# Optimization experiments

Measured on AMD Instinct MI355X. Metric: run time of the kernel, lower is better.

The kernel has to match this reference:

```python
import jax, jax.numpy as jnp
import numpy as np

N = 100000
E = 1600000
F_IN = 64
F_OUT = 64
C = 1.0
MIN_NORM = 1e-15
BALL_EPS = 4e-3  # float32 eps in HGCN PoincareBall.proj


def _norm(x):
    return jnp.clip(jnp.linalg.norm(x, axis=-1, keepdims=True), MIN_NORM)


def artanh(x):
    return jnp.arctanh(jnp.clip(x, -1.0 + 1e-7, 1.0 - 1e-7))


def proj(x, c):
    # project back onto the Poincare ball of curvature -c
    norm = _norm(x)
    maxnorm = (1.0 - BALL_EPS) / jnp.sqrt(c)
    return jnp.where(norm > maxnorm, x / norm * maxnorm, x)


def mobius_matvec(m, x, c):
    sqrt_c = jnp.sqrt(c)
    x_norm = _norm(x)
    mx = x @ m.T
    mx_norm = _norm(mx)
    res = jnp.tanh(mx_norm / x_norm * artanh(sqrt_c * x_norm)) * mx / (mx_norm * sqrt_c)
    zero_mx = jnp.all(mx == 0, axis=-1, keepdims=True)
    return jnp.where(zero_mx, jnp.zeros_like(res), res)


def expmap0(u, c):
    sqrt_c = jnp.sqrt(c)
    u_norm = _norm(u)
    return jnp.tanh(sqrt_c * u_norm) * u / (sqrt_c * u_norm)


def mobius_add(x, y, c):
    x2 = jnp.sum(x * x, axis=-1, keepdims=True)
    y2 = jnp.sum(y * y, axis=-1, keepdims=True)
    xy = jnp.sum(x * y, axis=-1, keepdims=True)
    num = (1.0 + 2.0 * c * xy + c * y2) * x + (1.0 - c * x2) * y
    denom = 1.0 + 2.0 * c * xy + c * c * x2 * y2
    return num / jnp.clip(denom, MIN_NORM)


def hyp_linear(x, W, b, c):
    res = proj(mobius_matvec(W, x, c), c)
    if b is not None:
        hyp_bias = proj(expmap0(b[None, :], c), c)
        res = proj(mobius_add(res, hyp_bias, c), c)
    return res


def scatter_mean(edge_index, x, n):
    # mean of source features over edges landing at each target node; 0 if isolated
    src, dst = edge_index[0], edge_index[1]
    s = jax.ops.segment_sum(x[src], dst, num_segments=n)
    cnt = jax.ops.segment_sum(jnp.ones((src.shape[0], 1), x.dtype), dst, num_segments=n)
    return s / jnp.clip(cnt, 1.0)


def setup_inputs() -> dict:
    key = jax.random.key(0)
    ks = jax.random.split(key, 9)
    glorot = 1.0 / np.sqrt(F_IN)
    return {
        "x": jax.random.normal(ks[0], (N, F_IN), dtype=jnp.float32) * 0.1,
        "W_pos": jax.random.uniform(ks[1], (F_OUT, F_IN), jnp.float32, -glorot, glorot),
        "W_pos_cc": jax.random.uniform(ks[2], (F_OUT, F_IN), jnp.float32, -glorot, glorot),
        "b_pos_cc": jax.random.uniform(ks[3], (F_OUT,), jnp.float32, -glorot, glorot),
        "W_neg": jax.random.uniform(ks[4], (F_OUT, F_IN), jnp.float32, -glorot, glorot),
        "W_neg_cc": jax.random.uniform(ks[5], (F_OUT, F_IN), jnp.float32, -glorot, glorot),
        "b_neg_cc": jax.random.uniform(ks[6], (F_OUT,), jnp.float32, -glorot, glorot),
        "pos_edge_index": jax.random.randint(ks[7], (2, E), 0, N, dtype=jnp.int64) if jax.config.jax_enable_x64 else jax.random.randint(ks[7], (2, E), 0, N, dtype=jnp.int32),
        "neg_edge_index": jax.random.randint(ks[8], (2, E), 0, N, dtype=jnp.int32),
    }


def reference(x, W_pos, W_pos_cc, b_pos_cc, W_neg, W_neg_cc, b_neg_cc, pos_edge_index, neg_edge_index):
    n = x.shape[0]
    # first_aggr=True branch of HSignedConv.forward
    agg_pos = scatter_mean(pos_edge_index, x, n)          # [N, F_IN]
    out_pos = hyp_linear(agg_pos, W_pos, None, C)
    out_pos = out_pos + hyp_linear(x, W_pos_cc, b_pos_cc, C)
    agg_neg = scatter_mean(neg_edge_index, x, n)
    out_neg = hyp_linear(agg_neg, W_neg, None, C)
    out_neg = out_neg + hyp_linear(x, W_neg_cc, b_neg_cc, C)
    return jnp.concatenate([out_pos, out_neg], axis=-1)  # [N, 2*F_OUT]
```

## Files before the change

### kernel.cpp

```cpp
#include <hip/hip_runtime.h>
#include <math.h>

#define NN 100000
#define BSZ 256
#define NB 391
#define NB2 782
constexpr float MAXNORM_C = 0.996f;
constexpr float MINNORM_C = 1e-15f;

__global__ void prep_transpose(const float* __restrict__ Wp, const float* __restrict__ Wpc,
                               const float* __restrict__ Wn, const float* __restrict__ Wnc,
                               float* __restrict__ wt) {
    int idx = blockIdx.x * 256 + threadIdx.x;
    int m = idx >> 12;
    int k = (idx >> 6) & 63;
    int j = idx & 63;
    const float* W = (m == 0) ? Wp : (m == 1) ? Wpc : (m == 2) ? Wn : Wnc;
    wt[idx] = W[j * 64 + k];
}

__device__ inline float wave_sum64(float v) {
    #pragma unroll
    for (int m = 32; m >= 1; m >>= 1) v += __shfl_xor(v, m, 64);
    return v;
}

__global__ void prep_bias(const float* __restrict__ bp, const float* __restrict__ bn,
                          float* __restrict__ hb) {
    int l = threadIdx.x;
    #pragma unroll
    for (int h = 0; h < 2; ++h) {
        float u = (h ? bn : bp)[l];
        float norm = fmaxf(sqrtf(wave_sum64(u * u)), MINNORM_C);
        float s = tanhf(norm) / norm;
        float v = s * u;
        float vn = fmaxf(sqrtf(wave_sum64(v * v)), MINNORM_C);
        if (vn > MAXNORM_C) v *= MAXNORM_C / vn;
        float y2 = wave_sum64(v * v);
        hb[h * 65 + l] = v;
        if (l == 0) hb[h * 65 + 64] = y2;
    }
}

__global__ __launch_bounds__(256) void bucket_count(
    const int* __restrict__ pei, int E1,
    const int* __restrict__ nei, int E2,
    int* __restrict__ gcnt) {
    __shared__ int h[NB2];
    int tid = threadIdx.x;
    for (int i = tid; i < NB2; i += 256) h[i] = 0;
    __syncthreads();
    int tot = E1 + E2;
    int base = blockIdx.x * 8192;
    #pragma unroll 4
    for (int k = 0; k < 32; ++k) {
        int idx = base + k * 256 + tid;
        if (idx < tot) {
            int half = idx >= E1;
            int e = idx - (half ? E1 : 0);
            const int* ei = half ? nei : pei;
            int E = half ? E2 : E1;
            int dst = ei[E + e];
            atomicAdd(&h[half * NB + (dst >> 8)], 1);
        }
    }
    __syncthreads();
    for (int i = tid; i < NB2; i += 256) {
        int c = h[i];
        if (c) atomicAdd(&gcnt[i], c);
    }
}

__global__ void bucket_scan(const int* __restrict__ gcnt, int* __restrict__ goffs,
                            int* __restrict__ gcursor) {
    __shared__ int tmp[256];
    int tid = threadIdx.x;
    int base = tid * 4;
    int items[4];
    int s = 0;
    #pragma unroll
    for (int i = 0; i < 4; ++i) {
        items[i] = (base + i < NB2) ? gcnt[base + i] : 0;
        s += items[i];
    }
    tmp[tid] = s;
    __syncthreads();
    for (int off = 1; off < 256; off <<= 1) {
        int v = (tid >= off) ? tmp[tid - off] : 0;
        __syncthreads();
        tmp[tid] += v;
        __syncthreads();
    }
    int run = tmp[tid] - s;
    #pragma unroll
    for (int i = 0; i < 4; ++i) {
        if (base + i < NB2) { goffs[base + i] = run; gcursor[base + i] = run; }
        run += items[i];
    }
}

__global__ __launch_bounds__(256) void bucket_scatter(
    const int* __restrict__ pei, int E1,
    const int* __restrict__ nei, int E2,
    int* __restrict__ gcursor, int* __restrict__ packed) {
    __shared__ int h[NB2];
    __shared__ int hb[NB2];
    int tid = threadIdx.x;
    for (int i = tid; i < NB2; i += 256) h[i] = 0;
    __syncthreads();
    int tot = E1 + E2;
    int base = blockIdx.x * 8192;
    #pragma unroll 4
    for (int k = 0; k < 32; ++k) {
        int idx = base + k * 256 + tid;
        if (idx < tot) {
            int half = idx >= E1;
            int e = idx - (half ? E1 : 0);
            const int* ei = half ? nei : pei;
            int E = half ? E2 : E1;
            int dst = ei[E + e];
            atomicAdd(&h[half * NB + (dst >> 8)], 1);
        }
    }
    __syncthreads();
    for (int i = tid; i < NB2; i += 256) {
        int c = h[i];
        hb[i] = c ? atomicAdd(&gcursor[i], c) : 0;
    }
    __syncthreads();
    for (int i = tid; i < NB2; i += 256) h[i] = 0;
    __syncthreads();
    #pragma unroll 4
    for (int k = 0; k < 32; ++k) {
        int idx = base + k * 256 + tid;
        if (idx < tot) {
            int half = idx >= E1;
            int e = idx - (half ? E1 : 0);
            const int* ei = half ? nei : pei;
            int E = half ? E2 : E1;
            int src = ei[e];
            int dst = ei[E + e];
            int b = half * NB + (dst >> 8);
            int r = atomicAdd(&h[b], 1);
            packed[hb[b] + r] = (src << 8) | (dst & 255);
        }
    }
}

__global__ __launch_bounds__(256) void node_sort(
    const int* __restrict__ goffs, const int* __restrict__ gcnt,
    const int* __restrict__ packed,
    int* __restrict__ esrc, int* __restrict__ ndeg, int* __restrict__ noffs) {
    __shared__ int h[256];
    __shared__ int sc[256];
    int tid = threadIdx.x;
    int bucket = blockIdx.x;
    int start = goffs[bucket];
    int cnt = gcnt[bucket];
    h[tid] = 0;
    __syncthreads();
    for (int i = start + tid; i < start + cnt; i += 256)
        atomicAdd(&h[packed[i] & 255], 1);
    __syncthreads();
    int deg = h[tid];
    sc[tid] = deg;
    __syncthreads();
    for (int off = 1; off < 256; off <<= 1) {
        int v = (tid >= off) ? sc[tid - off] : 0;
        __syncthreads();
        sc[tid] += v;
        __syncthreads();
    }
    int excl = sc[tid] - deg;
    int half = bucket >= NB;
    int node = (bucket - (half ? NB : 0)) * BSZ + tid;
    if (node < NN) {
        ndeg[half * NN + node] = deg;
        noffs[half * NN + node] = start + excl;
    }
    h[tid] = excl;
    __syncthreads();
    for (int i = start + tid; i < start + cnt; i += 256) {
        int p = packed[i];
        int r = atomicAdd(&h[p & 255], 1);
        esrc[start + r] = p >> 8;
    }
}

__global__ __launch_bounds__(256) void gather_kernel(
    const int* __restrict__ noffs, const int* __restrict__ ndeg,
    const int* __restrict__ esrc, const float* __restrict__ x,
    float* __restrict__ out) {
    int wid = (blockIdx.x * 256 + threadIdx.x) >> 6;
    int lane = threadIdx.x & 63;
    if (wid >= 2 * NN) return;
    int half = wid >= NN;
    int node = wid - (half ? NN : 0);
    int start = noffs[wid];
    int deg = ndeg[wid];
    float acc = 0.f;
    for (int b = 0; b < deg; b += 64) {
        int n = min(64, deg - b);
        int s_l = (b + lane < deg) ? esrc[start + b + lane] : 0;
        int i = 0;
        for (; i + 4 <= n; i += 4) {
            int a0 = __shfl(s_l, i, 64), a1 = __shfl(s_l, i + 1, 64);
            int a2 = __shfl(s_l, i + 2, 64), a3 = __shfl(s_l, i + 3, 64);
            float v0 = x[a0 * 64 + lane], v1 = x[a1 * 64 + lane];
            float v2 = x[a2 * 64 + lane], v3 = x[a3 * 64 + lane];
            acc += (v0 + v1) + (v2 + v3);
        }
        for (; i < n; ++i) acc += x[__shfl(s_l, i, 64) * 64 + lane];
    }
    float m = acc / fmaxf((float)deg, 1.f);
    out[(size_t)node * 128 + half * 64 + lane] = m;
}

__device__ __attribute__((always_inline)) inline void mm1(
        const float* p, const float4* wl, float (&m)[64], float& vn2out) {
    #pragma unroll
    for (int j = 0; j < 64; ++j) m[j] = 0.f;
    float vn2 = 0.f;
    #pragma unroll 1
    for (int k0 = 0; k0 < 64; k0 += 4) {
        float4 a = *(const float4*)(p + k0);
        vn2 = fmaf(a.x, a.x, fmaf(a.y, a.y, fmaf(a.z, a.z, fmaf(a.w, a.w, vn2))));
        const float4* wk = wl + k0 * 16;
        #pragma unroll
        for (int j4 = 0; j4 < 16; ++j4) {
            float4 w0 = wk[j4];
            float4 w1 = wk[16 + j4];
            float4 w2 = wk[32 + j4];
            float4 w3 = wk[48 + j4];
            int j = j4 * 4;
            m[j+0] = fmaf(a.x,w0.x, fmaf(a.y,w1.x, fmaf(a.z,w2.x, fmaf(a.w,w3.x, m[j+0]))));
            m[j+1] = fmaf(a.x,w0.y, fmaf(a.y,w1.y, fmaf(a.z,w2.y, fmaf(a.w,w3.y, m[j+1]))));
            m[j+2] = fmaf(a.x,w0.z, fmaf(a.y,w1.z, fmaf(a.z,w2.z, fmaf(a.w,w3.z, m[j+2]))));
            m[j+3] = fmaf(a.x,w0.w, fmaf(a.y,w1.w, fmaf(a.z,w2.w, fmaf(a.w,w3.w, m[j+3]))));
        }
    }
    vn2out = vn2;
}

__device__ __attribute__((always_inline)) inline void mob_scale_proj(
        float (&m)[64], float vn2) {
    float mn2 = 0.f;
    #pragma unroll
    for (int j = 0; j < 64; ++j) mn2 = fmaf(m[j], m[j], mn2);
    float xnorm = fmaxf(sqrtf(vn2), MINNORM_C);
    float mnorm = fmaxf(sqrtf(mn2), MINNORM_C);
    float z = fminf(xnorm, 1.0f - 1e-7f);
    float art = 0.5f * logf((1.0f + z) / (1.0f - z));
    float t = tanhf(mnorm / xnorm * art);
    float scale = (mn2 == 0.f) ? 0.f : (t / mnorm);
    #pragma unroll
    for (int j = 0; j < 64; ++j) m[j] *= scale;
    float rn2 = 0.f;
    #pragma unroll
    for (int j = 0; j < 64; ++j) rn2 = fmaf(m[j], m[j], rn2);
    float rnorm = fmaxf(sqrtf(rn2), MINNORM_C);
    float f = (rnorm > MAXNORM_C) ? (MAXNORM_C / rnorm) : 1.0f;
    #pragma unroll
    for (int j = 0; j < 64; ++j) m[j] *= f;
}

__device__ __attribute__((always_inline)) inline float bias_addf(
        float (&m)[64], const float* hbv) {
    float x2 = 0.f, xy = 0.f;
    #pragma unroll
    for (int j = 0; j < 64; ++j) {
        float h = hbv[j];
        x2 = fmaf(m[j], m[j], x2);
        xy = fmaf(m[j], h, xy);
    }
    float y2 = hbv[64];
    float A = 1.f + 2.f * xy + y2;
    float B = 1.f - x2;
    float den = 1.f + 2.f * xy + x2 * y2;
    float dinv = 1.f / fmaxf(den, MINNORM_C);
    float rn2 = 0.f;
    #pragma unroll
    for (int j = 0; j < 64; ++j) {
        float r = (A * m[j] + B * hbv[j]) * dinv;
        m[j] = r;
        rn2 = fmaf(r, r, rn2);
    }
    float rnorm = fmaxf(sqrtf(rn2), MINNORM_C);
    return (rnorm > MAXNORM_C) ? (MAXNORM_C / rnorm) : 1.0f;
}

__global__ __launch_bounds__(256, 2) void finalize_kernel(
    const float* __restrict__ x,
    const float* __restrict__ wt,
    const float* __restrict__ hb,
    float* __restrict__ out) {
    __shared__ float4 wlds[2048];
    __shared__ __align__(16) float hbs[68];
    int tid = threadIdx.x;
    int half = blockIdx.x & 1;

    const float4* wsrc = (const float4*)(wt + half * 8192);
    #pragma unroll
    for (int i = 0; i < 8; ++i) wlds[i * 256 + tid] = wsrc[i * 256 + tid];
    if (tid < 65) hbs[tid] = hb[half * 65 + tid];
    __syncthreads();

    int node = (blockIdx.x >> 1) * 256 + tid;
    bool valid = node < NN;
    int nc = valid ? node : NN - 1;
    float* op = out + (size_t)nc * 128 + half * 64;

    {
        float m[64];
        float vn2;
        mm1(op, wlds, m, vn2);
        mob_scale_proj(m, vn2);
        if (valid) {
            #pragma unroll
            for (int k0 = 0; k0 < 64; k0 += 4)
                *(float4*)(op + k0) = make_float4(m[k0], m[k0+1], m[k0+2], m[k0+3]);
        }
    }

    {
        float m[64];
        float vn2;
        mm1(x + (size_t)nc * 64, wlds + 1024, m, vn2);
        mob_scale_proj(m, vn2);
        float f = bias_addf(m, hbs);
        if (valid) {
            #pragma unroll
            for (int k0 = 0; k0 < 64; k0 += 4) {
                float4 a = *(const float4*)(op + k0);
                a.x += m[k0 + 0] * f;
                a.y += m[k0 + 1] * f;
                a.z += m[k0 + 2] * f;
                a.w += m[k0 + 3] * f;
                *(float4*)(op + k0) = a;
            }
        }
    }
}

extern "C" void kernel_launch(void* const* d_in, const int* in_sizes, int n_in,
                              void* d_out, int out_size, void* d_ws, size_t ws_size,
                              hipStream_t stream) {
    const float* x   = (const float*)d_in[0];
    const float* Wp  = (const float*)d_in[1];
    const float* Wpc = (const float*)d_in[2];
    const float* bp  = (const float*)d_in[3];
    const float* Wn  = (const float*)d_in[4];
    const float* Wnc = (const float*)d_in[5];
    const float* bn  = (const float*)d_in[6];
    const int* pei = (const int*)d_in[7];
    const int* nei = (const int*)d_in[8];
    float* out = (float*)d_out;

    int E1 = in_sizes[7] / 2;
    int E2 = in_sizes[8] / 2;
    int tot = E1 + E2;

    int*   gcnt    = (int*)d_ws;
    int*   goffs   = gcnt + NB2;
    int*   gcursor = goffs + NB2;
    int*   ndeg    = gcursor + NB2 + 2;
    int*   noffs   = ndeg + 2 * NN;
    float* hbp     = (float*)(noffs + 2 * NN);
    float* wt      = hbp + 192;
    int*   packed  = (int*)(wt + 16384);
    int*   esrc    = packed + tot;

    hipMemsetAsync(gcnt, 0, NB2 * sizeof(int), stream);

    prep_transpose<<<64, 256, 0, stream>>>(Wp, Wpc, Wn, Wnc, wt);
    prep_bias<<<1, 64, 0, stream>>>(bp, bn, hbp);

    int nblk = (tot + 8191) / 8192;
    bucket_count<<<nblk, 256, 0, stream>>>(pei, E1, nei, E2, gcnt);
    bucket_scan<<<1, 256, 0, stream>>>(gcnt, goffs, gcursor);
    bucket_scatter<<<nblk, 256, 0, stream>>>(pei, E1, nei, E2, gcursor, packed);
    node_sort<<<NB2, 256, 0, stream>>>(goffs, gcnt, packed, esrc, ndeg, noffs);

    gather_kernel<<<(2 * NN * 64 + 255) / 256, 256, 0, stream>>>(noffs, ndeg, esrc, x, out);

    int fblocks = 2 * ((NN + 255) / 256);
    finalize_kernel<<<fblocks, 256, 0, stream>>>(x, wt, hbp, out);
}
```

Before: 423.9 us.

## Read second weight matrix via scalar loads and merge output writes

The finalize kernel now stages only the first weight matrix in LDS. The second matrix is read straight from global memory with wave-uniform addresses, which the compiler can turn into scalar loads. Both hyperbolic-linear results are kept in registers and written to the output once, so the intermediate store and reload of the output row go away. The cost is 128 live accumulator floats per thread, which raises register pressure and may cause spills or lower occupancy under the 256x2 launch bounds.

```diff
diff --git a/kernel.cpp b/kernel.cpp
--- a/kernel.cpp
+++ b/kernel.cpp
@@ -216,7 +216,7 @@
     out[(size_t)node * 128 + half * 64 + lane] = m;
 }
 
-__device__ __attribute__((always_inline)) inline void mm1(
+__device__ __attribute__((always_inline)) inline void mm1_lds(
         const float* p, const float4* wl, float (&m)[64], float& vn2out) {
     #pragma unroll
     for (int j = 0; j < 64; ++j) m[j] = 0.f;
@@ -242,6 +242,28 @@
     vn2out = vn2;
 }
 
+__device__ __attribute__((always_inline)) inline void mm1_s(
+        const float* p, const float* __restrict__ wtm, float (&m)[64], float& vn2out) {
+    #pragma unroll
+    for (int j = 0; j < 64; ++j) m[j] = 0.f;
+    float vn2 = 0.f;
+    for (int k0 = 0; k0 < 64; k0 += 4) {
+        float4 a = *(const float4*)(p + k0);
+        vn2 = fmaf(a.x, a.x, fmaf(a.y, a.y, fmaf(a.z, a.z, fmaf(a.w, a.w, vn2))));
+        const float* w0 = wtm + k0 * 64;
+        #pragma unroll
+        for (int j = 0; j < 64; ++j) {
+            float mm = m[j];
+            mm = fmaf(a.x, w0[j],        mm);
+            mm = fmaf(a.y, w0[64 + j],   mm);
+            mm = fmaf(a.z, w0[128 + j],  mm);
+            mm = fmaf(a.w, w0[192 + j],  mm);
+            m[j] = mm;
+        }
+    }
+    vn2out = vn2;
+}
+
 __device__ __attribute__((always_inline)) inline void mob_scale_proj(
         float (&m)[64], float vn2) {
     float mn2 = 0.f;
@@ -275,13 +297,13 @@
     }
     float y2 = hbv[64];
     float A = 1.f + 2.f * xy + y2;
-    float B = 1.f - x2;
+    float Bc = 1.f - x2;
     float den = 1.f + 2.f * xy + x2 * y2;
     float dinv = 1.f / fmaxf(den, MINNORM_C);
     float rn2 = 0.f;
     #pragma unroll
     for (int j = 0; j < 64; ++j) {
-        float r = (A * m[j] + B * hbv[j]) * dinv;
+        float r = (A * m[j] + Bc * hbv[j]) * dinv;
         m[j] = r;
         rn2 = fmaf(r, r, rn2);
     }
@@ -294,14 +316,14 @@
     const float* __restrict__ wt,
     const float* __restrict__ hb,
     float* __restrict__ out) {
-    __shared__ float4 wlds[2048];
+    __shared__ float4 wlds[1024];
     __shared__ __align__(16) float hbs[68];
     int tid = threadIdx.x;
     int half = blockIdx.x & 1;
 
     const float4* wsrc = (const float4*)(wt + half * 8192);
     #pragma unroll
-    for (int i = 0; i < 8; ++i) wlds[i * 256 + tid] = wsrc[i * 256 + tid];
+    for (int i = 0; i < 4; ++i) wlds[i * 256 + tid] = wsrc[i * 256 + tid];
     if (tid < 65) hbs[tid] = hb[half * 65 + tid];
     __syncthreads();
 
@@ -310,34 +332,24 @@
     int nc = valid ? node : NN - 1;
     float* op = out + (size_t)nc * 128 + half * 64;
 
-    {
-        float m[64];
-        float vn2;
-        mm1(op, wlds, m, vn2);
-        mob_scale_proj(m, vn2);
-        if (valid) {
-            #pragma unroll
-            for (int k0 = 0; k0 < 64; k0 += 4)
-                *(float4*)(op + k0) = make_float4(m[k0], m[k0+1], m[k0+2], m[k0+3]);
-        }
-    }
-
-    {
-        float m[64];
-        float vn2;
-        mm1(x + (size_t)nc * 64, wlds + 1024, m, vn2);
-        mob_scale_proj(m, vn2);
-        float f = bias_addf(m, hbs);
-        if (valid) {
-            #pragma unroll
-            for (int k0 = 0; k0 < 64; k0 += 4) {
-                float4 a = *(const float4*)(op + k0);
-                a.x += m[k0 + 0] * f;
-                a.y += m[k0 + 1] * f;
-                a.z += m[k0 + 2] * f;
-                a.w += m[k0 + 3] * f;
-                *(float4*)(op + k0) = a;
-            }
+    float mA[64];
+    float vnA;
+    mm1_lds(op, wlds, mA, vnA);
+    mob_scale_proj(mA, vnA);
+
+    float mB[64];
+    float vnB;
+    mm1_s(x + (size_t)nc * 64, wt + half * 8192 + 4096, mB, vnB);
+    mob_scale_proj(mB, vnB);
+    float f = bias_addf(mB, hbs);
+
+    if (valid) {
+        #pragma unroll
+        for (int k0 = 0; k0 < 64; k0 += 4) {
+            *(float4*)(op + k0) = make_float4(mA[k0+0] + mB[k0+0] * f,
+                                              mA[k0+1] + mB[k0+1] * f,
+                                              mA[k0+2] + mB[k0+2] * f,
+                                              mA[k0+3] + mB[k0+3] * f);
         }
     }
 }
```

Result: no change. 424.3 us (+0.1%).
